# Kernel optimization log

Hardware: AMD Instinct MI355X
Metric: run time of the kernel (lower is better)

The kernel has to match this reference:

```python
import jax, jax.numpy as jnp
import numpy as np

B, C, H, W = 2, 512, 64, 64
G = 32          # GroupNorm groups
EPS = 1e-6


def setup_inputs() -> dict:
    key = jax.random.key(0)
    ks = jax.random.split(key, 10)
    s = 1.0 / np.sqrt(C)
    return {
        "x": jax.random.normal(ks[0], (B, C, H, W), dtype=jnp.float32),
        "gn_w": jnp.ones((C,), jnp.float32),
        "gn_b": jnp.zeros((C,), jnp.float32),
        "wq": jax.random.normal(ks[1], (C, C), jnp.float32) * s,
        "bq": jnp.zeros((C,), jnp.float32),
        "wk": jax.random.normal(ks[2], (C, C), jnp.float32) * s,
        "bk": jnp.zeros((C,), jnp.float32),
        "wv": jax.random.normal(ks[3], (C, C), jnp.float32) * s,
        "bv": jnp.zeros((C,), jnp.float32),
        "wo": jax.random.normal(ks[4], (C, C), jnp.float32) * s,
        "bo": jnp.zeros((C,), jnp.float32),
    }


def reference(x, gn_w, gn_b, wq, bq, wk, bk, wv, bv, wo, bo):
    b, c, h, w = x.shape
    n = h * w
    # GroupNorm(32, eps=1e-6, affine)
    xg = x.reshape(b, G, c // G, h, w)
    mu = xg.mean(axis=(2, 3, 4), keepdims=True)
    var = ((xg - mu) ** 2).mean(axis=(2, 3, 4), keepdims=True)
    hn = ((xg - mu) * jax.lax.rsqrt(var + EPS)).reshape(b, c, h, w)
    hn = hn * gn_w[None, :, None, None] + gn_b[None, :, None, None]
    # 1x1 convs == per-pixel linear over channels; tokens: b n c
    hf = hn.reshape(b, c, n)
    q = jnp.einsum('oc,bcn->bno', wq, hf) + bq  # [b, n, c]
    k = jnp.einsum('oc,bcn->bno', wk, hf) + bk
    v = jnp.einsum('oc,bcn->bno', wv, hf) + bv
    scale = jnp.asarray(c, x.dtype) ** -0.5
    att = jax.nn.softmax(jnp.einsum('bic,bjc->bij', q, k) * scale, axis=-1)
    o = jnp.einsum('bij,bjc->bic', att, v)      # [b, n, c]
    out = jnp.einsum('oc,bnc->bno', wo, o) + bo # proj_out
    return x + out.transpose(0, 2, 1).reshape(b, c, h, w)
```

## Files before the change

### kernel.cpp

```cpp
#include <hip/hip_runtime.h>
#include <hip/hip_bf16.h>


typedef float f32x4 __attribute__((ext_vector_type(4)));
typedef __bf16 bf16x8 __attribute__((ext_vector_type(8)));

typedef const __attribute__((address_space(1))) unsigned char* gas_p;
typedef __attribute__((address_space(3))) unsigned char* las_p;

__device__ __forceinline__ void gload_lds16(const void* g, void* l) {
  __builtin_amdgcn_global_load_lds((gas_p)g, (las_p)l, 16, 0, 0);
}

__global__ __launch_bounds__(256) void prelude_k(
    const float* __restrict__ wq, const float* __restrict__ wk,
    const float* __restrict__ wv, const float* __restrict__ wo,
    __hip_bfloat16* __restrict__ wqkb, __hip_bfloat16* __restrict__ wvb,
    __hip_bfloat16* __restrict__ wob, const float* __restrict__ bq,
    const float* __restrict__ bk, float* __restrict__ bqk,
    const float* __restrict__ x, float* __restrict__ stats) {
  int bid = blockIdx.x;
  if (bid < 4096) {
    const float* src;
    __hip_bfloat16* dst;
    if (bid < 1024)      { src = wq; dst = wqkb; }
    else if (bid < 2048) { src = wk; dst = wqkb + 262144; }
    else if (bid < 3072) { src = wv; dst = wvb; }
    else                 { src = wo; dst = wob; }
    int i = (bid & 1023) * 256 + threadIdx.x;
    dst[i] = __float2bfloat16(src[i]);
    return;
  }
  if (bid < 4160) {
    int bg = bid - 4096;
    const float4* p = (const float4*)(x + (size_t)bg * 65536);
    float s = 0.f, s2 = 0.f;
    for (int i = threadIdx.x; i < 16384; i += 256) {
      float4 v = p[i];
      s  += v.x + v.y + v.z + v.w;
      s2 += v.x * v.x + v.y * v.y + v.z * v.z + v.w * v.w;
    }
#pragma unroll
    for (int off = 32; off > 0; off >>= 1) {
      s  += __shfl_xor(s, off);
      s2 += __shfl_xor(s2, off);
    }
    __shared__ float rs[4], rs2[4];
    int wid = threadIdx.x >> 6, lane = threadIdx.x & 63;
    if (lane == 0) { rs[wid] = s; rs2[wid] = s2; }
    __syncthreads();
    if (threadIdx.x == 0) {
      float S  = rs[0] + rs[1] + rs[2] + rs[3];
      float S2 = rs2[0] + rs2[1] + rs2[2] + rs2[3];
      float mean = S * (1.f / 65536.f);
      float var  = S2 * (1.f / 65536.f) - mean * mean;
      stats[bg * 2]     = mean;
      stats[bg * 2 + 1] = rsqrtf(var + 1e-6f);
    }
    return;
  }
  for (int j = threadIdx.x; j < 1024; j += 256)
    bqk[j] = (j < 512) ? bq[j] : bk[j - 512];
}

__global__ __launch_bounds__(256) void gn_apply_k(const float* __restrict__ x,
                                                  const float* __restrict__ stats,
                                                  const float* __restrict__ gw,
                                                  const float* __restrict__ gb,
                                                  __hip_bfloat16* __restrict__ hf) {
  int c0 = blockIdx.x * 64, n0 = blockIdx.y * 64, b = blockIdx.z;
  __shared__ float tile[64][65];
  int tx = threadIdx.x & 63, ty = threadIdx.x >> 6;
  const float* xb = x + ((size_t)(b * 512 + c0)) * 4096 + n0;
#pragma unroll
  for (int i = 0; i < 64; i += 4) {
    int cl = i + ty;
    int c  = c0 + cl;
    float mean = stats[(b * 32 + (c >> 4)) * 2];
    float rstd = stats[(b * 32 + (c >> 4)) * 2 + 1];
    float v = xb[(size_t)cl * 4096 + tx];
    tile[cl][tx] = (v - mean) * rstd * gw[c] + gb[c];
  }
  __syncthreads();
  __hip_bfloat16* o = hf + ((size_t)(b * 4096 + n0)) * 512 + c0;
#pragma unroll
  for (int i = 0; i < 64; i += 4) {
    int nl = i + ty;
    o[(size_t)nl * 512 + tx] = __float2bfloat16(tile[tx][nl]);
  }
}

__global__ __launch_bounds__(256) void sum32_k(const float* __restrict__ psums,
                                               float* __restrict__ rowsum) {
  int i = blockIdx.x * 256 + threadIdx.x;
  float s = 0.f;
#pragma unroll
  for (int j = 0; j < 32; j++) s += psums[(size_t)j * 8192 + i];
  rowsum[i] = s;
}

__global__ __launch_bounds__(256, 4) void qkv_k(
    const __hip_bfloat16* __restrict__ hf, const __hip_bfloat16* __restrict__ wqk,
    const __hip_bfloat16* __restrict__ wv, const float* __restrict__ bqk,
    const float* __restrict__ bv, __hip_bfloat16* __restrict__ qk,
    __hip_bfloat16* __restrict__ vT) {
  bool isV = blockIdx.x >= 8;
  int m0 = isV ? (blockIdx.x - 8) * 128 : blockIdx.y * 128;
  int n0 = isV ? blockIdx.y * 128 : blockIdx.x * 128;
  const __hip_bfloat16* A  = isV ? wv : hf;
  const __hip_bfloat16* Bm = isV ? hf : wqk;

  __shared__ __align__(16) unsigned char smem[34816];
  __hip_bfloat16* As  = (__hip_bfloat16*)smem;
  __hip_bfloat16* Bs  = As + 8192;
  __hip_bfloat16* epi = (__hip_bfloat16*)smem;

  int tid  = threadIdx.x;
  int wvx  = tid >> 6, lane = tid & 63;
  int wr   = (wvx >> 1) * 64, wc = (wvx & 1) * 64;
  int quad = lane >> 4, l16 = lane & 15;

  int srow = wvx * 32 + (lane >> 2);
  int scol = (lane & 3) * 8;
  const __hip_bfloat16* gA0 = A  + (size_t)(m0 + srow) * 512 + scol;
  const __hip_bfloat16* gA1 = gA0 + (size_t)16 * 512;
  const __hip_bfloat16* gB0 = Bm + (size_t)(n0 + srow) * 512 + scol;
  const __hip_bfloat16* gB1 = gB0 + (size_t)16 * 512;

  auto stage = [&](int kk, int bsel) {
    int lb = bsel * 4096 + wvx * 1024;
    gload_lds16(gA0 + kk, &As[lb]);
    gload_lds16(gA1 + kk, &As[lb + 512]);
    gload_lds16(gB0 + kk, &Bs[lb]);
    gload_lds16(gB1 + kk, &Bs[lb + 512]);
  };

  f32x4 acc[4][4] = {};
  stage(0, 0);
  for (int kt = 0; kt < 16; kt++) {
    __syncthreads();
    if (kt + 1 < 16) stage((kt + 1) << 5, (kt + 1) & 1);
    const __hip_bfloat16* Ab = &As[(kt & 1) * 4096];
    const __hip_bfloat16* Bb = &Bs[(kt & 1) * 4096];
    bf16x8 af[4], bfr[4];
#pragma unroll
    for (int i = 0; i < 4; i++)
      af[i] = *(const bf16x8*)&Ab[(wr + i * 16 + l16) * 32 + quad * 8];
#pragma unroll
    for (int j = 0; j < 4; j++)
      bfr[j] = *(const bf16x8*)&Bb[(wc + j * 16 + l16) * 32 + quad * 8];
#pragma unroll
    for (int i = 0; i < 4; i++)
#pragma unroll
      for (int j = 0; j < 4; j++)
        acc[i][j] = __builtin_amdgcn_mfma_f32_16x16x32_bf16(af[i], bfr[j],
                                                            acc[i][j], 0, 0, 0);
  }

  float bj[4], bm[4][4];
  if (!isV) {
#pragma unroll
    for (int j = 0; j < 4; j++) bj[j] = bqk[n0 + wc + j * 16 + l16];
  } else {
#pragma unroll
    for (int i = 0; i < 4; i++)
#pragma unroll
      for (int r = 0; r < 4; r++)
        bm[i][r] = bv[m0 + wr + i * 16 + quad * 4 + r];
  }
  __syncthreads();
#pragma unroll
  for (int i = 0; i < 4; i++)
#pragma unroll
    for (int j = 0; j < 4; j++)
#pragma unroll
      for (int r = 0; r < 4; r++) {
        int ml = wr + i * 16 + quad * 4 + r;
        int nl = wc + j * 16 + l16;
        float v = acc[i][j][r] + (isV ? bm[i][r] : bj[j]);
        epi[ml * 136 + nl] = __float2bfloat16(v);
      }
  __syncthreads();
  int mr = tid >> 1, h = tid & 1;
  const __hip_bfloat16* rowp = &epi[mr * 136 + h * 64];
  if (!isV) {
    __hip_bfloat16* o = qk + (size_t)(m0 + mr) * 1024 + n0 + h * 64;
#pragma unroll
    for (int c = 0; c < 8; c++)
      *(uint4*)(o + c * 8) = *(const uint4*)(rowp + c * 8);
  } else {
    int b = (n0 + h * 64) >> 12, t = (n0 + h * 64) & 4095;
    __hip_bfloat16* o = vT + ((size_t)(b * 512 + m0 + mr)) * 4096 + t;
#pragma unroll
    for (int c = 0; c < 8; c++)
      *(uint4*)(o + c * 8) = *(const uint4*)(rowp + c * 8);
  }
}

template <int MODE>
__global__ __launch_bounds__(256, 4) void gemm_bt_k(
    const __hip_bfloat16* __restrict__ A, const __hip_bfloat16* __restrict__ Bm,
    void* __restrict__ Cout, const float* __restrict__ bias,
    const float* __restrict__ resid, float* __restrict__ rowsum, int Kc,
    int lda, int ldb, int ldc, float scale, long sAz, long sBz, long sCz,
    int kspl) {
  int bx, by, bz;
  if (MODE == 3) {
    int f = blockIdx.x;
    int xcd = f & 7, s = f >> 3;
    bx = s & 3;
    int g = xcd + 8 * (s >> 2);
    by = g & 31;
    bz = g >> 5;
  } else {
    bx = blockIdx.x; by = blockIdx.y; bz = blockIdx.z;
  }
  int bb = bz / kspl, ks = bz - bb * kspl;
  A  += (size_t)bb * sAz + (size_t)ks * Kc;
  Bm += (size_t)bb * sBz + (size_t)ks * Kc;
  size_t cbase = (size_t)bz * sCz;
  int m0 = by * 128, n0 = bx * 128;

  __shared__ __align__(16) unsigned char smem[34816];
  __hip_bfloat16* As  = (__hip_bfloat16*)smem;
  __hip_bfloat16* Bs  = As + 8192;
  __hip_bfloat16* epi = (__hip_bfloat16*)smem;
  float* psum2 = (float*)(smem + 32768);

  int tid  = threadIdx.x;
  int wv   = tid >> 6, lane = tid & 63;
  int wr   = (wv >> 1) * 64, wc = (wv & 1) * 64;
  int quad = lane >> 4, l16 = lane & 15;

  int srow = wv * 32 + (lane >> 2);
  int scol = (lane & 3) * 8;
  const __hip_bfloat16* gA0 = A  + (size_t)(m0 + srow) * lda + scol;
  const __hip_bfloat16* gA1 = gA0 + (size_t)16 * lda;
  const __hip_bfloat16* gB0 = Bm + (size_t)(n0 + srow) * ldb + scol;
  const __hip_bfloat16* gB1 = gB0 + (size_t)16 * ldb;

  auto stage = [&](int kk, int bsel) {
    int lb = bsel * 4096 + wv * 1024;
    gload_lds16(gA0 + kk, &As[lb]);
    gload_lds16(gA1 + kk, &As[lb + 512]);
    gload_lds16(gB0 + kk, &Bs[lb]);
    gload_lds16(gB1 + kk, &Bs[lb + 512]);
  };

  int KT = Kc >> 5;
  f32x4 acc[4][4] = {};
  stage(0, 0);
  for (int kt = 0; kt < KT; kt++) {
    __syncthreads();
    if (kt + 1 < KT) stage((kt + 1) << 5, (kt + 1) & 1);
    const __hip_bfloat16* Ab = &As[(kt & 1) * 4096];
    const __hip_bfloat16* Bb = &Bs[(kt & 1) * 4096];
    bf16x8 af[4], bfr[4];
#pragma unroll
    for (int i = 0; i < 4; i++)
      af[i] = *(const bf16x8*)&Ab[(wr + i * 16 + l16) * 32 + quad * 8];
#pragma unroll
    for (int j = 0; j < 4; j++)
      bfr[j] = *(const bf16x8*)&Bb[(wc + j * 16 + l16) * 32 + quad * 8];
#pragma unroll
    for (int i = 0; i < 4; i++)
#pragma unroll
      for (int j = 0; j < 4; j++)
        acc[i][j] = __builtin_amdgcn_mfma_f32_16x16x32_bf16(af[i], bfr[j],
                                                            acc[i][j], 0, 0, 0);
  }

  if (MODE == 2) {
    float s[4][4];
#pragma unroll
    for (int i = 0; i < 4; i++)
#pragma unroll
      for (int r = 0; r < 4; r++) s[i][r] = 0.f;
    __hip_bfloat16* o = (__hip_bfloat16*)Cout;
#pragma unroll
    for (int i = 0; i < 4; i++)
#pragma unroll
      for (int j = 0; j < 4; j++)
#pragma unroll
        for (int r = 0; r < 4; r++) {
          int m = m0 + wr + i * 16 + quad * 4 + r;
          int n = n0 + wc + j * 16 + l16;
          float v = __expf(acc[i][j][r] * scale);
          o[cbase + (size_t)m * ldc + n] = __float2bfloat16(v);
          s[i][r] += v;
        }
#pragma unroll
    for (int off = 1; off < 16; off <<= 1)
#pragma unroll
      for (int i = 0; i < 4; i++)
#pragma unroll
        for (int r = 0; r < 4; r++) s[i][r] += __shfl_xor(s[i][r], off);
    if (l16 == 0) {
#pragma unroll
      for (int i = 0; i < 4; i++)
#pragma unroll
        for (int r = 0; r < 4; r++)
          psum2[(wv & 1) * 128 + wr + i * 16 + quad * 4 + r] = s[i][r];
    }
    __syncthreads();
    if (tid < 128) {
      float v = psum2[tid] + psum2[128 + tid];
      rowsum[(size_t)bx * 8192 + bb * 4096 + m0 + tid] = v;
    }
    return;
  }

  float pre[4][4];
  if (MODE == 6) {
#pragma unroll
    for (int i = 0; i < 4; i++)
#pragma unroll
      for (int r = 0; r < 4; r++)
        pre[i][r] = bias[m0 + wr + i * 16 + quad * 4 + r];
  }
  __syncthreads();
#pragma unroll
  for (int i = 0; i < 4; i++)
#pragma unroll
    for (int j = 0; j < 4; j++)
#pragma unroll
      for (int r = 0; r < 4; r++) {
        int ml = wr + i * 16 + quad * 4 + r;
        int nl = wc + j * 16 + l16;
        float v = acc[i][j][r];
        if (MODE == 6) v += pre[i][r];
        epi[ml * 136 + nl] = __float2bfloat16(v);
      }
  __syncthreads();
  int mr = tid >> 1, h = tid & 1;
  const __hip_bfloat16* rowp = &epi[mr * 136 + h * 64];
  size_t obase = cbase + (size_t)(m0 + mr) * ldc + n0 + h * 64;
  if (MODE == 3) {
    __hip_bfloat16* o = (__hip_bfloat16*)Cout + obase;
#pragma unroll
    for (int c = 0; c < 8; c++)
      *(uint4*)(o + c * 8) = *(const uint4*)(rowp + c * 8);
  } else {
    float* o = (float*)Cout;
#pragma unroll
    for (int c = 0; c < 8; c++) {
      bf16x8 val = *(const bf16x8*)(rowp + c * 8);
      size_t idx = obase + c * 8;
      float4 r0 = *(const float4*)&resid[idx];
      float4 r1 = *(const float4*)&resid[idx + 4];
      float4 o0, o1;
      o0.x = r0.x + (float)val[0]; o0.y = r0.y + (float)val[1];
      o0.z = r0.z + (float)val[2]; o0.w = r0.w + (float)val[3];
      o1.x = r1.x + (float)val[4]; o1.y = r1.y + (float)val[5];
      o1.z = r1.z + (float)val[6]; o1.w = r1.w + (float)val[7];
      *(float4*)&o[idx] = o0;
      *(float4*)&o[idx + 4] = o1;
    }
  }
}

__global__ __launch_bounds__(256) void reduce_k(const __hip_bfloat16* __restrict__ part,
                                                const float* __restrict__ rowsum,
                                                __hip_bfloat16* __restrict__ obuf) {
  size_t i8 = (size_t)blockIdx.x * 256 + threadIdx.x;
  size_t perb = (size_t)4096 * 512 / 8;
  size_t b = i8 / perb, r = i8 - b * perb;
  float inv = 1.f / rowsum[b * 4096 + (r >> 6)];
  float acc[8] = {};
#pragma unroll
  for (int ks = 0; ks < 2; ks++) {
    bf16x8 v = ((const bf16x8*)part)[(b * 2 + ks) * perb + r];
#pragma unroll
    for (int l = 0; l < 8; l++) acc[l] += (float)v[l];
  }
  bf16x8 o;
#pragma unroll
  for (int l = 0; l < 8; l++) o[l] = (__bf16)(acc[l] * inv);
  ((bf16x8*)obuf)[b * perb + r] = o;
}

extern "C" void kernel_launch(void* const* d_in, const int* in_sizes, int n_in,
                              void* d_out, int out_size, void* d_ws,
                              size_t ws_size, hipStream_t stream) {
  const float* xp  = (const float*)d_in[0];
  const float* gwp = (const float*)d_in[1];
  const float* gbp = (const float*)d_in[2];
  const float* wqp = (const float*)d_in[3];
  const float* bqp = (const float*)d_in[4];
  const float* wkp = (const float*)d_in[5];
  const float* bkp = (const float*)d_in[6];
  const float* wvp = (const float*)d_in[7];
  const float* bvp = (const float*)d_in[8];
  const float* wop = (const float*)d_in[9];
  const float* bop = (const float*)d_in[10];
  float* outp = (float*)d_out;

  char* w = (char*)d_ws;
  size_t off = 0;
  auto alloc = [&](size_t bytes) {
    void* p = w + off;
    off += (bytes + 255) & ~(size_t)255;
    return p;
  };
  float* stats         = (float*)alloc(64 * 2 * sizeof(float));
  __hip_bfloat16* hf   = (__hip_bfloat16*)alloc((size_t)2 * 4096 * 512 * 2);
  __hip_bfloat16* wqkb = (__hip_bfloat16*)alloc((size_t)1024 * 512 * 2);
  __hip_bfloat16* wvb  = (__hip_bfloat16*)alloc((size_t)512 * 512 * 2);
  __hip_bfloat16* wob  = (__hip_bfloat16*)alloc((size_t)512 * 512 * 2);
  float* bqk           = (float*)alloc(1024 * sizeof(float));
  float* rowsum        = (float*)alloc(8192 * sizeof(float));
  float* psums         = (float*)alloc((size_t)32 * 8192 * sizeof(float));
  __hip_bfloat16* qk   = (__hip_bfloat16*)alloc((size_t)2 * 4096 * 1024 * 2);
  __hip_bfloat16* vT   = (__hip_bfloat16*)alloc((size_t)2 * 512 * 4096 * 2);
  __hip_bfloat16* obuf = (__hip_bfloat16*)alloc((size_t)2 * 4096 * 512 * 2);
  __hip_bfloat16* part = (__hip_bfloat16*)alloc((size_t)4 * 4096 * 512 * 2);
  __hip_bfloat16* Sbuf = (__hip_bfloat16*)alloc((size_t)2 * 4096 * 4096 * 2);

  prelude_k<<<4161, 256, 0, stream>>>(wqp, wkp, wvp, wop, wqkb, wvb, wob,
                                      bqp, bkp, bqk, xp, stats);

  gn_apply_k<<<dim3(8, 64, 2), 256, 0, stream>>>(xp, stats, gwp, gbp, hf);

  qkv_k<<<dim3(12, 64, 1), 256, 0, stream>>>(hf, wqkb, wvb, bqk, bvp, qk, vT);

  gemm_bt_k<2><<<dim3(32, 32, 2), 256, 0, stream>>>(
      qk, qk + 512, Sbuf, nullptr, nullptr, psums, 512, 1024, 1024, 4096,
      0.044194173824159216f, (long)4096 * 1024, (long)4096 * 1024,
      (long)4096 * 4096, 1);

  sum32_k<<<32, 256, 0, stream>>>(psums, rowsum);

  gemm_bt_k<3><<<dim3(512, 1, 1), 256, 0, stream>>>(
      Sbuf, vT, part, nullptr, nullptr, nullptr, 2048, 4096, 4096, 512, 1.f,
      (long)4096 * 4096, (long)512 * 4096, (long)4096 * 512, 2);

  reduce_k<<<2048, 256, 0, stream>>>(part, rowsum, obuf);

  gemm_bt_k<6><<<dim3(32, 4, 2), 256, 0, stream>>>(
      wob, obuf, outp, bop, xp, nullptr, 512, 512, 512, 4096, 1.f,
      0, (long)4096 * 512, (long)512 * 4096, 1);
}
```

Before: 270.0 us.

## Add dedicated PV GEMM kernel with BK=64 swizzled LDS and fold rowsum reduction

Replaces the generic MODE 3 GEMM for P·V with a specialized kernel that uses 64-wide K tiles, double-buffered in 64KB of LDS with an XOR swizzle to avoid bank conflicts, and the same XCD-aware block mapping. The QK^T exp epilogue now goes through the LDS staging buffer for coalesced stores and computes row sums from the bf16-rounded values. The separate sum32 kernel is removed, and reduce_k sums the 32 partial row sums with wave shuffles. This trades lower occupancy in the PV kernel for deeper K tiles and one fewer launch.

```diff
diff --git a/kernel.cpp b/kernel.cpp
--- a/kernel.cpp
+++ b/kernel.cpp
@@ -90,15 +90,6 @@
   }
 }
 
-__global__ __launch_bounds__(256) void sum32_k(const float* __restrict__ psums,
-                                               float* __restrict__ rowsum) {
-  int i = blockIdx.x * 256 + threadIdx.x;
-  float s = 0.f;
-#pragma unroll
-  for (int j = 0; j < 32; j++) s += psums[(size_t)j * 8192 + i];
-  rowsum[i] = s;
-}
-
 __global__ __launch_bounds__(256, 4) void qkv_k(
     const __hip_bfloat16* __restrict__ hf, const __hip_bfloat16* __restrict__ wqk,
     const __hip_bfloat16* __restrict__ wv, const float* __restrict__ bqk,
@@ -204,17 +195,7 @@
     const float* __restrict__ resid, float* __restrict__ rowsum, int Kc,
     int lda, int ldb, int ldc, float scale, long sAz, long sBz, long sCz,
     int kspl) {
-  int bx, by, bz;
-  if (MODE == 3) {
-    int f = blockIdx.x;
-    int xcd = f & 7, s = f >> 3;
-    bx = s & 3;
-    int g = xcd + 8 * (s >> 2);
-    by = g & 31;
-    bz = g >> 5;
-  } else {
-    bx = blockIdx.x; by = blockIdx.y; bz = blockIdx.z;
-  }
+  int bx = blockIdx.x, by = blockIdx.y, bz = blockIdx.z;
   int bb = bz / kspl, ks = bz - bb * kspl;
   A  += (size_t)bb * sAz + (size_t)ks * Kc;
   Bm += (size_t)bb * sBz + (size_t)ks * Kc;
@@ -225,7 +206,6 @@
   __hip_bfloat16* As  = (__hip_bfloat16*)smem;
   __hip_bfloat16* Bs  = As + 8192;
   __hip_bfloat16* epi = (__hip_bfloat16*)smem;
-  float* psum2 = (float*)(smem + 32768);
 
   int tid  = threadIdx.x;
   int wv   = tid >> 6, lane = tid & 63;
@@ -270,46 +250,6 @@
                                                             acc[i][j], 0, 0, 0);
   }
 
-  if (MODE == 2) {
-    float s[4][4];
-#pragma unroll
-    for (int i = 0; i < 4; i++)
-#pragma unroll
-      for (int r = 0; r < 4; r++) s[i][r] = 0.f;
-    __hip_bfloat16* o = (__hip_bfloat16*)Cout;
-#pragma unroll
-    for (int i = 0; i < 4; i++)
-#pragma unroll
-      for (int j = 0; j < 4; j++)
-#pragma unroll
-        for (int r = 0; r < 4; r++) {
-          int m = m0 + wr + i * 16 + quad * 4 + r;
-          int n = n0 + wc + j * 16 + l16;
-          float v = __expf(acc[i][j][r] * scale);
-          o[cbase + (size_t)m * ldc + n] = __float2bfloat16(v);
-          s[i][r] += v;
-        }
-#pragma unroll
-    for (int off = 1; off < 16; off <<= 1)
-#pragma unroll
-      for (int i = 0; i < 4; i++)
-#pragma unroll
-        for (int r = 0; r < 4; r++) s[i][r] += __shfl_xor(s[i][r], off);
-    if (l16 == 0) {
-#pragma unroll
-      for (int i = 0; i < 4; i++)
-#pragma unroll
-        for (int r = 0; r < 4; r++)
-          psum2[(wv & 1) * 128 + wr + i * 16 + quad * 4 + r] = s[i][r];
-    }
-    __syncthreads();
-    if (tid < 128) {
-      float v = psum2[tid] + psum2[128 + tid];
-      rowsum[(size_t)bx * 8192 + bb * 4096 + m0 + tid] = v;
-    }
-    return;
-  }
-
   float pre[4][4];
   if (MODE == 6) {
 #pragma unroll
@@ -328,18 +268,26 @@
         int ml = wr + i * 16 + quad * 4 + r;
         int nl = wc + j * 16 + l16;
         float v = acc[i][j][r];
-        if (MODE == 6) v += pre[i][r];
+        if (MODE == 2) v = __expf(v * scale);
+        else v += pre[i][r];
         epi[ml * 136 + nl] = __float2bfloat16(v);
       }
   __syncthreads();
   int mr = tid >> 1, h = tid & 1;
   const __hip_bfloat16* rowp = &epi[mr * 136 + h * 64];
   size_t obase = cbase + (size_t)(m0 + mr) * ldc + n0 + h * 64;
-  if (MODE == 3) {
+  if (MODE == 2) {
+    float s = 0.f;
     __hip_bfloat16* o = (__hip_bfloat16*)Cout + obase;
 #pragma unroll
-    for (int c = 0; c < 8; c++)
-      *(uint4*)(o + c * 8) = *(const uint4*)(rowp + c * 8);
+    for (int c = 0; c < 8; c++) {
+      bf16x8 val = *(const bf16x8*)(rowp + c * 8);
+#pragma unroll
+      for (int l = 0; l < 8; l++) s += (float)val[l];
+      *(uint4*)(o + c * 8) = *(const uint4*)&val;
+    }
+    s += __shfl_xor(s, 1);
+    if (h == 0) rowsum[(size_t)bx * 8192 + bb * 4096 + m0 + mr] = s;
   } else {
     float* o = (float*)Cout;
 #pragma unroll
@@ -359,13 +307,103 @@
   }
 }
 
-__global__ __launch_bounds__(256) void reduce_k(const __hip_bfloat16* __restrict__ part,
-                                                const float* __restrict__ rowsum,
-                                                __hip_bfloat16* __restrict__ obuf) {
+__global__ __launch_bounds__(256, 2) void pv_k(
+    const __hip_bfloat16* __restrict__ P, const __hip_bfloat16* __restrict__ vT,
+    __hip_bfloat16* __restrict__ part) {
+  int f = blockIdx.x;
+  int xcd = f & 7, s = f >> 3;
+  int bx = s & 3;
+  int g = xcd + 8 * (s >> 2);
+  int by = g & 31, bz = g >> 5;
+  int bb = bz >> 1, ks = bz & 1;
+  const __hip_bfloat16* A = P  + (size_t)bb * 4096 * 4096 + (size_t)ks * 2048;
+  const __hip_bfloat16* B = vT + (size_t)bb * 512 * 4096 + (size_t)ks * 2048;
+  size_t cbase = (size_t)bz * 4096 * 512;
+  int m0 = by * 128, n0 = bx * 128;
+
+  __shared__ __align__(16) unsigned char smem[65536];
+  __hip_bfloat16* As  = (__hip_bfloat16*)smem;
+  __hip_bfloat16* Bs  = (__hip_bfloat16*)(smem + 32768);
+  __hip_bfloat16* epi = (__hip_bfloat16*)smem;
+
+  int tid = threadIdx.x, wv = tid >> 6, lane = tid & 63;
+  int wr = (wv >> 1) * 64, wc = (wv & 1) * 64;
+  int quad = lane >> 4, l16 = lane & 15;
+
+  int srow = wv * 32 + (lane >> 3);
+  int scol = ((lane & 7) ^ (lane >> 3)) * 8;
+  const __hip_bfloat16* gA = A + (size_t)(m0 + srow) * 4096 + scol;
+  const __hip_bfloat16* gB = B + (size_t)(n0 + srow) * 4096 + scol;
+
+  auto stage = [&](int kk, int bsel) {
+    __hip_bfloat16* la = &As[bsel * 8192 + wv * 2048];
+    __hip_bfloat16* lb = &Bs[bsel * 8192 + wv * 2048];
+#pragma unroll
+    for (int c = 0; c < 4; c++) {
+      gload_lds16(gA + kk + (size_t)(c * 8) * 4096, la + c * 512);
+      gload_lds16(gB + kk + (size_t)(c * 8) * 4096, lb + c * 512);
+    }
+  };
+
+  f32x4 acc[4][4] = {};
+  stage(0, 0);
+  for (int kt = 0; kt < 32; kt++) {
+    __syncthreads();
+    if (kt + 1 < 32) stage((kt + 1) << 6, (kt + 1) & 1);
+    const __hip_bfloat16* Ab = &As[(kt & 1) * 8192];
+    const __hip_bfloat16* Bb = &Bs[(kt & 1) * 8192];
+#pragma unroll
+    for (int ksub = 0; ksub < 2; ksub++) {
+      bf16x8 af[4], bfr[4];
+#pragma unroll
+      for (int i = 0; i < 4; i++) {
+        int r = wr + i * 16 + l16;
+        af[i] = *(const bf16x8*)&Ab[r * 64 + ((ksub * 4 + quad) ^ (r & 7)) * 8];
+      }
+#pragma unroll
+      for (int j = 0; j < 4; j++) {
+        int r = wc + j * 16 + l16;
+        bfr[j] = *(const bf16x8*)&Bb[r * 64 + ((ksub * 4 + quad) ^ (r & 7)) * 8];
+      }
+#pragma unroll
+      for (int i = 0; i < 4; i++)
+#pragma unroll
+        for (int j = 0; j < 4; j++)
+          acc[i][j] = __builtin_amdgcn_mfma_f32_16x16x32_bf16(af[i], bfr[j],
+                                                              acc[i][j], 0, 0, 0);
+    }
+  }
+
+  __syncthreads();
+#pragma unroll
+  for (int i = 0; i < 4; i++)
+#pragma unroll
+    for (int j = 0; j < 4; j++)
+#pragma unroll
+      for (int r = 0; r < 4; r++)
+        epi[(wr + i * 16 + quad * 4 + r) * 136 + wc + j * 16 + l16] =
+            __float2bfloat16(acc[i][j][r]);
+  __syncthreads();
+  int mr = tid >> 1, h = tid & 1;
+  const __hip_bfloat16* rowp = &epi[mr * 136 + h * 64];
+  __hip_bfloat16* o = part + cbase + (size_t)(m0 + mr) * 512 + n0 + h * 64;
+#pragma unroll
+  for (int c = 0; c < 8; c++)
+    *(uint4*)(o + c * 8) = *(const uint4*)(rowp + c * 8);
+}
+
+__global__ __launch_bounds__(256) void reduce_k(
+    const __hip_bfloat16* __restrict__ part, const float* __restrict__ psums,
+    __hip_bfloat16* __restrict__ obuf) {
   size_t i8 = (size_t)blockIdx.x * 256 + threadIdx.x;
   size_t perb = (size_t)4096 * 512 / 8;
   size_t b = i8 / perb, r = i8 - b * perb;
-  float inv = 1.f / rowsum[b * 4096 + (r >> 6)];
+  int t = (int)(r >> 6);
+  int lane = threadIdx.x & 63;
+  float ps = psums[(size_t)(lane & 31) * 8192 + b * 4096 + t];
+#pragma unroll
+  for (int off = 1; off < 32; off <<= 1) ps += __shfl_xor(ps, off);
+  float inv = 1.f / ps;
   float acc[8] = {};
 #pragma unroll
   for (int ks = 0; ks < 2; ks++) {
@@ -408,7 +446,6 @@
   __hip_bfloat16* wvb  = (__hip_bfloat16*)alloc((size_t)512 * 512 * 2);
   __hip_bfloat16* wob  = (__hip_bfloat16*)alloc((size_t)512 * 512 * 2);
   float* bqk           = (float*)alloc(1024 * sizeof(float));
-  float* rowsum        = (float*)alloc(8192 * sizeof(float));
   float* psums         = (float*)alloc((size_t)32 * 8192 * sizeof(float));
   __hip_bfloat16* qk   = (__hip_bfloat16*)alloc((size_t)2 * 4096 * 1024 * 2);
   __hip_bfloat16* vT   = (__hip_bfloat16*)alloc((size_t)2 * 512 * 4096 * 2);
@@ -428,13 +465,9 @@
       0.044194173824159216f, (long)4096 * 1024, (long)4096 * 1024,
       (long)4096 * 4096, 1);
 
-  sum32_k<<<32, 256, 0, stream>>>(psums, rowsum);
-
-  gemm_bt_k<3><<<dim3(512, 1, 1), 256, 0, stream>>>(
-      Sbuf, vT, part, nullptr, nullptr, nullptr, 2048, 4096, 4096, 512, 1.f,
-      (long)4096 * 4096, (long)512 * 4096, (long)4096 * 512, 2);
-
-  reduce_k<<<2048, 256, 0, stream>>>(part, rowsum, obuf);
+  pv_k<<<512, 256, 0, stream>>>(Sbuf, vT, part);
+
+  reduce_k<<<2048, 256, 0, stream>>>(part, psums, obuf);
 
   gemm_bt_k<6><<<dim3(32, 4, 2), 256, 0, stream>>>(
       wob, obuf, outp, bop, xp, nullptr, 512, 512, 512, 4096, 1.f,
```

New measurement: 269.2 us. No clear change (-0.3%).
